# Performance work log

Measured on AMD Instinct MI355X. Metric: run time of the kernel, lower is better.

Reference implementation:

```python
import jax, jax.numpy as jnp
import numpy as np

NEG_SLOPE = 0.2


def _gat(x, W, a_src, a_dst, bias, src, dst, nonself, N):
    # PyG GATConv (eval mode): h = x @ W -> [N,H,C]; per-edge scores with
    # LeakyReLU, softmax over incoming edges per target node (self loops
    # re-added after removing any existing ones), weighted scatter-add.
    H, C = a_src.shape
    h = (x @ W).reshape(N, H, C)
    al_s = jnp.einsum('nhc,hc->nh', h, a_src)  # [N,H]
    al_d = jnp.einsum('nhc,hc->nh', h, a_dst)
    e = jax.nn.leaky_relu(al_s[src] + al_d[dst], NEG_SLOPE)  # [E,H]
    e = jnp.where(nonself[:, None], e, -jnp.inf)  # drop input self loops
    e_self = jax.nn.leaky_relu(al_s + al_d, NEG_SLOPE)  # added self loops [N,H]
    m = jnp.maximum(jax.ops.segment_max(e, dst, num_segments=N), e_self)
    w = jnp.exp(e - m[dst])  # masked edges -> 0
    w_self = jnp.exp(e_self - m)
    num = jax.ops.segment_sum(w[:, :, None] * h[src], dst, num_segments=N)
    num = num + w_self[:, :, None] * h
    den = jax.ops.segment_sum(w, dst, num_segments=N) + w_self
    return (num / den[:, :, None]).reshape(N, H * C) + bias


def setup_inputs() -> dict:
    N, E = 100000, 3200000
    key = jax.random.key(0)
    ks = jax.random.split(key, 20)
    s = 0.1
    return {
        'x1': jax.random.normal(ks[0], (N, 7), jnp.float32),
        'x2': jax.random.normal(ks[1], (N, 1), jnp.float32),
        'edge_index': jax.random.randint(ks[2], (2, E), 0, N, jnp.int64)
            if jax.config.jax_enable_x64 else jax.random.randint(ks[2], (2, E), 0, N, jnp.int32),
        'num_nodes': N,
        'lin1_w': s * jax.random.normal(ks[3], (1, 7), jnp.float32),
        'lin1_b': s * jax.random.normal(ks[4], (1,), jnp.float32),
        'lin2_w': s * jax.random.normal(ks[5], (1, 8), jnp.float32),
        'W1': s * jax.random.normal(ks[6], (1, 32), jnp.float32),
        'a_src1': s * jax.random.normal(ks[7], (8, 4), jnp.float32),
        'a_dst1': s * jax.random.normal(ks[8], (8, 4), jnp.float32),
        'b1': s * jax.random.normal(ks[9], (32,), jnp.float32),
        'W2': s * jax.random.normal(ks[10], (32, 16), jnp.float32),
        'a_src2': s * jax.random.normal(ks[11], (4, 4), jnp.float32),
        'a_dst2': s * jax.random.normal(ks[12], (4, 4), jnp.float32),
        'b2': s * jax.random.normal(ks[13], (16,), jnp.float32),
        'W3': s * jax.random.normal(ks[14], (16, 8), jnp.float32),
        'a_src3': s * jax.random.normal(ks[15], (2, 4), jnp.float32),
        'a_dst3': s * jax.random.normal(ks[16], (2, 4), jnp.float32),
        'b3': s * jax.random.normal(ks[17], (8,), jnp.float32),
    }


def reference(x1, x2, edge_index, num_nodes, lin1_w, lin1_b, lin2_w,
              W1, a_src1, a_dst1, b1, W2, a_src2, a_dst2, b2,
              W3, a_src3, a_dst3, b3):
    N = num_nodes
    src, dst = edge_index[0], edge_index[1]
    nonself = src != dst
    # init score + 3 GAT layers (dropouts inactive in eval mode)
    h0 = jax.nn.relu(x1 @ lin1_w.T + lin1_b)  # [N,1]
    x3 = jax.nn.relu(_gat(h0, W1, a_src1, a_dst1, b1, src, dst, nonself, N))
    x4 = jax.nn.relu(_gat(x3, W2, a_src2, a_dst2, b2, src, dst, nonself, N))
    x6 = jax.nn.relu(_gat(x4, W3, a_src3, a_dst3, b3, src, dst, nonself, N))  # [N,8]
    # Row-normalized adjacency with diagonal filled to 1 (sparse form of the
    # original dense Adj): Adj[i,j] = 1/deg[i] on edges (i!=j) and diagonal.
    ns = nonself.astype(x6.dtype)
    deg = 1.0 + jax.ops.segment_sum(ns, src, num_segments=N)  # [N]
    # local score: rowsum(Adj * (x6 x6^T))
    dots = jnp.sum(x6[src] * x6[dst], axis=-1) * ns  # [E]
    local = (jax.ops.segment_sum(dots, src, num_segments=N)
             + jnp.sum(x6 * x6, axis=-1)) / deg  # [N]
    # global score: lin2(Adj @ x6)
    R3 = (jax.ops.segment_sum(x6[dst] * ns[:, None], src, num_segments=N)
          + x6) / deg[:, None]  # [N,8]
    return local[:, None] + R3 @ lin2_w.T  # [N,1]
```

## Files before the change

kernel.cpp:

```cpp
#include <hip/hip_runtime.h>
#include <hip/hip_fp16.h>
#include <math.h>

static constexpr float NEG_SLOPE = 0.2f;
static constexpr int P      = 256;
static constexpr int CAP    = 14000;
static constexpr int CHSZ   = 4096;

__device__ __forceinline__ float lrelu(float x) { return x > 0.0f ? x : NEG_SLOPE * x; }

__device__ __forceinline__ void dm(int x, unsigned int mg, int npr, int& r, int& lk) {
    r = (int)__umulhi((unsigned int)x, mg);
    lk = x - r * npr;
    if (lk >= npr) { lk -= npr; ++r; }
    else if (lk < 0) { lk += npr; --r; }
}

union H8 { int4 i4; __half2 h2[4]; };

__device__ __forceinline__ void h8_to_f(int4 v, float* o) {
    H8 u; u.i4 = v;
#pragma unroll
    for (int k = 0; k < 4; ++k) {
        float2 f = __half22float2(u.h2[k]);
        o[2 * k] = f.x; o[2 * k + 1] = f.y;
    }
}

__device__ __forceinline__ int4 f_to_h8(const float* s) {
    H8 u;
#pragma unroll
    for (int k = 0; k < 4; ++k)
        u.h2[k] = __float22half2_rn(make_float2(s[2 * k], s[2 * k + 1]));
    return u.i4;
}

__global__ __launch_bounds__(512) void part2_kernel(
    const int* __restrict__ src, const int* __restrict__ dst,
    int* __restrict__ gcount,
    unsigned int* __restrict__ stgd, unsigned int* __restrict__ stgs,
    int E, int npr, unsigned int mg)
{
    __shared__ int cntw[8 * P];
    __shared__ int base[P];
    __shared__ int pref[P];
    __shared__ int wsum[8];
    __shared__ unsigned int buf[CHSZ];
    __shared__ unsigned char rid[CHSZ];
    const int dir = blockIdx.x & 1;
    const int c = blockIdx.x >> 1;
    const int i0 = c * CHSZ;
    const int i1 = min(i0 + CHSZ, E);
    const int tot = i1 - i0;
    const int tid = threadIdx.x;
    const int lane = tid & 63, w = tid >> 6;
    const int* key = dir ? (src + i0) : (dst + i0);
    const int* val = dir ? (dst + i0) : (src + i0);
    unsigned int* stg = dir ? stgs : stgd;
    int* gc = gcount + dir * P;
    int* mycnt = cntw + w * P;
    for (int i = tid; i < 8 * P; i += 512) cntw[i] = 0;
    __syncthreads();
    const int nv = tot >> 2;
    const int4* k4 = (const int4*)key;
    for (int t = tid; t < nv; t += 512) {
        int4 k = k4[t];
        int r, lk;
        dm(k.x, mg, npr, r, lk); atomicAdd(&mycnt[r], 1);
        dm(k.y, mg, npr, r, lk); atomicAdd(&mycnt[r], 1);
        dm(k.z, mg, npr, r, lk); atomicAdd(&mycnt[r], 1);
        dm(k.w, mg, npr, r, lk); atomicAdd(&mycnt[r], 1);
    }
    for (int i = (nv << 2) + tid; i < tot; i += 512) {
        int r, lk;
        dm(key[i], mg, npr, r, lk);
        atomicAdd(&mycnt[r], 1);
    }
    __syncthreads();
    int cq[8];
    int tb = 0, x = 0;
    if (tid < P) {
#pragma unroll
        for (int q = 0; q < 8; ++q) { cq[q] = cntw[q * P + tid]; tb += cq[q]; }
        base[tid] = atomicAdd(&gc[tid], tb);
        x = tb;
#pragma unroll
        for (int off = 1; off < 64; off <<= 1) {
            int y = __shfl_up(x, off);
            if (lane >= off) x += y;
        }
        if (lane == 63) wsum[w] = x;
    }
    __syncthreads();
    if (tid < P) {
        int wpref = 0;
#pragma unroll
        for (int k = 0; k < 4; ++k) if (k < w) wpref += wsum[k];
        int ex = x + wpref - tb;
        pref[tid] = ex;
        int acc = ex;
#pragma unroll
        for (int q = 0; q < 8; ++q) { cntw[q * P + tid] = acc; acc += cq[q]; }
    }
    __syncthreads();
    int* mytick = cntw + w * P;
    for (int t = tid; t < nv; t += 512) {
        int4 k = k4[t];
        const int4* v4 = (const int4*)val;
        int4 v = v4[t];
        int r, lk, p;
        dm(k.x, mg, npr, r, lk); p = atomicAdd(&mytick[r], 1);
        buf[p] = ((unsigned int)lk << 17) | (unsigned int)v.x; rid[p] = (unsigned char)r;
        dm(k.y, mg, npr, r, lk); p = atomicAdd(&mytick[r], 1);
        buf[p] = ((unsigned int)lk << 17) | (unsigned int)v.y; rid[p] = (unsigned char)r;
        dm(k.z, mg, npr, r, lk); p = atomicAdd(&mytick[r], 1);
        buf[p] = ((unsigned int)lk << 17) | (unsigned int)v.z; rid[p] = (unsigned char)r;
        dm(k.w, mg, npr, r, lk); p = atomicAdd(&mytick[r], 1);
        buf[p] = ((unsigned int)lk << 17) | (unsigned int)v.w; rid[p] = (unsigned char)r;
    }
    for (int i = (nv << 2) + tid; i < tot; i += 512) {
        int r, lk;
        dm(key[i], mg, npr, r, lk);
        int p = atomicAdd(&mytick[r], 1);
        buf[p] = ((unsigned int)lk << 17) | (unsigned int)val[i];
        rid[p] = (unsigned char)r;
    }
    __syncthreads();
    for (int i = tid; i < tot; i += 512) {
        int r = (int)rid[i];
        int b = base[r] + (i - pref[r]);
        if (b < CAP) stg[(size_t)r * CAP + b] = buf[i];
    }
}

__global__ __launch_bounds__(512) void ebase_kernel(
    const int* __restrict__ gtot, int* __restrict__ ebase)
{
    __shared__ int sm[2 * P];
    int tid = threadIdx.x;
    int v = gtot[tid];
    sm[tid] = v;
    __syncthreads();
#pragma unroll
    for (int off = 1; off < P; off <<= 1) {
        int t = ((tid & (P - 1)) >= off) ? sm[tid - off] : 0;
        __syncthreads();
        sm[tid] += t;
        __syncthreads();
    }
    ebase[tid] = sm[tid] - v;
}

__global__ __launch_bounds__(512) void build_kernel(
    const unsigned int* __restrict__ stgd, const unsigned int* __restrict__ stgs,
    const int* __restrict__ gtot, const int* __restrict__ ebase,
    int* __restrict__ col_dst, int* __restrict__ col_src,
    int* __restrict__ deg_dst, int* __restrict__ deg_src,
    int* __restrict__ row_dst, int* __restrict__ row_src,
    int N, int npr)
{
    __shared__ int cntw[2 * 512];
    __shared__ int scn[512];
    __shared__ int outv[CAP];
    const int dir = blockIdx.x >> 8;
    const int r = blockIdx.x & (P - 1);
    const unsigned int* stg = (dir ? stgs : stgd) + (size_t)r * CAP;
    int tot = gtot[dir * P + r];
    if (tot > CAP) tot = CAP;
    const int n0 = r * npr;
    const int nb = min(npr, N - n0);
    const int tid = threadIdx.x;
    const int g = tid >> 8;
    int* mycnt = cntw + g * 512;
    cntw[tid] = 0; cntw[512 + tid] = 0;
    __syncthreads();
    for (int i = tid; i < tot; i += 512)
        atomicAdd(&mycnt[stg[i] >> 17], 1);
    __syncthreads();
    int c0 = cntw[tid], c1 = cntw[512 + tid];
    int v = c0 + c1;
    scn[tid] = v;
    __syncthreads();
#pragma unroll
    for (int off = 1; off < 512; off <<= 1) {
        int t = (tid >= off) ? scn[tid - off] : 0;
        __syncthreads();
        scn[tid] += t;
        __syncthreads();
    }
    int ex = scn[tid] - v;
    const int eb = ebase[dir * P + r];
    if (tid < nb) {
        (dir ? deg_src : deg_dst)[n0 + tid] = v;
        (dir ? row_src : row_dst)[n0 + tid] = eb + ex;
    }
    cntw[tid] = ex;
    cntw[512 + tid] = ex + c0;
    __syncthreads();
    for (int i = tid; i < tot; i += 512) {
        unsigned int w = stg[i];
        int t = atomicAdd(&mycnt[w >> 17], 1);
        outv[t] = (int)(w & 0x1FFFFu);
    }
    __syncthreads();
    int* col = (dir ? col_src : col_dst) + eb;
    for (int i = tid; i < tot; i += 512) col[i] = outv[i];
}

__global__ __launch_bounds__(256) void l1h0_kernel(
    const float* __restrict__ x1, const float* __restrict__ lin1_w,
    const float* __restrict__ lin1_b, float* __restrict__ h0, int N)
{
    int n = blockIdx.x * blockDim.x + threadIdx.x;
    if (n >= N) return;
    float acc = lin1_b[0];
#pragma unroll
    for (int k = 0; k < 7; ++k) acc = fmaf(x1[n * 7 + k], lin1_w[k], acc);
    h0[n] = fmaxf(acc, 0.0f);
}

__global__ __launch_bounds__(256) void gat_gather1_kernel(
    const int* __restrict__ row_start, const int* __restrict__ degv,
    const int* __restrict__ col, const float* __restrict__ h0,
    const float* __restrict__ W1, const float* __restrict__ a_src,
    const float* __restrict__ a_dst, const float* __restrict__ bias,
    const float* __restrict__ W2, int4* __restrict__ h2p, int N)
{
    int t = blockIdx.x * 256 + threadIdx.x;
    int n = t >> 3, lane = t & 7;
    if (n >= N) return;
    float cs[8], cd[8];
#pragma unroll
    for (int hd = 0; hd < 8; ++hd) {
        float s = 0.0f, d = 0.0f;
#pragma unroll
        for (int c = 0; c < 4; ++c) {
            s = fmaf(W1[hd * 4 + c], a_src[hd * 4 + c], s);
            d = fmaf(W1[hd * 4 + c], a_dst[hd * 4 + c], d);
        }
        cs[hd] = s; cd[hd] = d;
    }
    float h0n = h0[n];
    float wh[8], den[8], adn[8];
#pragma unroll
    for (int hd = 0; hd < 8; ++hd) {
        adn[hd] = h0n * cd[hd];
        if (lane == 0) {
            float w = __expf(lrelu(h0n * cs[hd] + adn[hd]));
            den[hd] = w; wh[hd] = w * h0n;
        } else { den[hd] = 0.0f; wh[hd] = 0.0f; }
    }
    int start = row_start[n];
    int end = start + degv[n];
    for (int e = start + lane; e < end; e += 8) {
        int s = col[e];
        if (s == n) continue;
        float hs = h0[s];
#pragma unroll
        for (int hd = 0; hd < 8; ++hd) {
            float w = __expf(lrelu(hs * cs[hd] + adn[hd]));
            den[hd] += w;
            wh[hd] = fmaf(w, hs, wh[hd]);
        }
    }
#pragma unroll
    for (int m = 1; m < 8; m <<= 1) {
#pragma unroll
        for (int hd = 0; hd < 8; ++hd) {
            den[hd] += __shfl_xor(den[hd], m);
            wh[hd]  += __shfl_xor(wh[hd], m);
        }
    }
    float fct = wh[lane] / den[lane];
    const float4 wv = ((const float4*)W1)[lane];
    const float4 bb = ((const float4*)bias)[lane];
    float xr[4];
    xr[0] = fmaxf(fmaf(fct, wv.x, bb.x), 0.0f);
    xr[1] = fmaxf(fmaf(fct, wv.y, bb.y), 0.0f);
    xr[2] = fmaxf(fmaf(fct, wv.z, bb.z), 0.0f);
    xr[3] = fmaxf(fmaf(fct, wv.w, bb.w), 0.0f);
    float pj[16];
#pragma unroll
    for (int j = 0; j < 16; ++j) pj[j] = 0.0f;
    const float* wbase = W2 + lane * 64;
#pragma unroll
    for (int c2 = 0; c2 < 4; ++c2) {
#pragma unroll
        for (int j = 0; j < 16; ++j)
            pj[j] = fmaf(xr[c2], wbase[c2 * 16 + j], pj[j]);
    }
#pragma unroll
    for (int m = 1; m < 8; m <<= 1) {
#pragma unroll
        for (int j = 0; j < 16; ++j) pj[j] += __shfl_xor(pj[j], m);
    }
    if (lane < 2) h2p[(size_t)n * 2 + lane] = f_to_h8(pj + lane * 8);
}

__global__ __launch_bounds__(256) void gat_gather2_kernel(
    const int* __restrict__ row_start, const int* __restrict__ degv,
    const int* __restrict__ col, const int4* __restrict__ hp,
    const float* __restrict__ a_src, const float* __restrict__ a_dst,
    const float* __restrict__ bias, const float* __restrict__ W3,
    int4* __restrict__ h3p, int N)
{
    int t = blockIdx.x * 256 + threadIdx.x;
    int n = t >> 3, lane = t & 7;
    if (n >= N) return;
    float As[16], Ad[16];
#pragma unroll
    for (int j = 0; j < 16; ++j) { As[j] = a_src[j]; Ad[j] = a_dst[j]; }
    float hn[16];
    h8_to_f(hp[(size_t)n * 2], hn);
    h8_to_f(hp[(size_t)n * 2 + 1], hn + 8);
    float ald[4];
#pragma unroll
    for (int hd = 0; hd < 4; ++hd) {
        float d = 0.0f;
#pragma unroll
        for (int c = 0; c < 4; ++c) d = fmaf(hn[hd * 4 + c], Ad[hd * 4 + c], d);
        ald[hd] = d;
    }
    float num[16], den[4];
    if (lane == 0) {
#pragma unroll
        for (int hd = 0; hd < 4; ++hd) {
            float a = 0.0f;
#pragma unroll
            for (int c = 0; c < 4; ++c) a = fmaf(hn[hd * 4 + c], As[hd * 4 + c], a);
            float w = __expf(lrelu(a + ald[hd]));
            den[hd] = w;
#pragma unroll
            for (int c = 0; c < 4; ++c) num[hd * 4 + c] = w * hn[hd * 4 + c];
        }
    } else {
#pragma unroll
        for (int j = 0; j < 16; ++j) num[j] = 0.0f;
#pragma unroll
        for (int hd = 0; hd < 4; ++hd) den[hd] = 0.0f;
    }
    int start = row_start[n];
    int end = start + degv[n];
    for (int e = start + lane; e < end; e += 8) {
        int s = col[e];
        if (s == n) continue;
        float hs[16];
        h8_to_f(hp[(size_t)s * 2], hs);
        h8_to_f(hp[(size_t)s * 2 + 1], hs + 8);
#pragma unroll
        for (int hd = 0; hd < 4; ++hd) {
            float a = 0.0f;
#pragma unroll
            for (int c = 0; c < 4; ++c) a = fmaf(hs[hd * 4 + c], As[hd * 4 + c], a);
            float w = __expf(lrelu(a + ald[hd]));
            den[hd] += w;
#pragma unroll
            for (int c = 0; c < 4; ++c) num[hd * 4 + c] = fmaf(w, hs[hd * 4 + c], num[hd * 4 + c]);
        }
    }
#pragma unroll
    for (int m = 1; m < 8; m <<= 1) {
#pragma unroll
        for (int hd = 0; hd < 4; ++hd) den[hd] += __shfl_xor(den[hd], m);
#pragma unroll
        for (int j = 0; j < 16; ++j) num[j] += __shfl_xor(num[j], m);
    }
    float invd[4];
#pragma unroll
    for (int hd = 0; hd < 4; ++hd) invd[hd] = 1.0f / den[hd];
    float pj[8];
#pragma unroll
    for (int j = 0; j < 8; ++j) pj[j] = 0.0f;
#pragma unroll
    for (int k = 0; k < 16; ++k) {
        float xk = fmaxf(fmaf(num[k], invd[k >> 2], bias[k]), 0.0f);
        const float* wrow = W3 + k * 8;
#pragma unroll
        for (int j = 0; j < 8; ++j) pj[j] = fmaf(xk, wrow[j], pj[j]);
    }
    if (lane == 0) h3p[n] = f_to_h8(pj);
}

__global__ __launch_bounds__(256) void gat_gather3_kernel(
    const int* __restrict__ row_start, const int* __restrict__ degv,
    const int* __restrict__ col, const int4* __restrict__ hp,
    const float* __restrict__ a_src, const float* __restrict__ a_dst,
    const float* __restrict__ bias, int4* __restrict__ x6p, int N)
{
    int t = blockIdx.x * 256 + threadIdx.x;
    int n = t >> 2, lane = t & 3;
    if (n >= N) return;
    float As[8], Ad[8];
#pragma unroll
    for (int j = 0; j < 8; ++j) { As[j] = a_src[j]; Ad[j] = a_dst[j]; }
    float hn[8];
    h8_to_f(hp[n], hn);
    float ald[2];
#pragma unroll
    for (int hd = 0; hd < 2; ++hd) {
        float d = 0.0f;
#pragma unroll
        for (int c = 0; c < 4; ++c) d = fmaf(hn[hd * 4 + c], Ad[hd * 4 + c], d);
        ald[hd] = d;
    }
    float num[8], den[2];
    if (lane == 0) {
#pragma unroll
        for (int hd = 0; hd < 2; ++hd) {
            float a = 0.0f;
#pragma unroll
            for (int c = 0; c < 4; ++c) a = fmaf(hn[hd * 4 + c], As[hd * 4 + c], a);
            float w = __expf(lrelu(a + ald[hd]));
            den[hd] = w;
#pragma unroll
            for (int c = 0; c < 4; ++c) num[hd * 4 + c] = w * hn[hd * 4 + c];
        }
    } else {
#pragma unroll
        for (int j = 0; j < 8; ++j) num[j] = 0.0f;
        den[0] = den[1] = 0.0f;
    }
    int start = row_start[n];
    int end = start + degv[n];
    for (int e = start + lane; e < end; e += 4) {
        int s = col[e];
        if (s == n) continue;
        float hs[8];
        h8_to_f(hp[s], hs);
#pragma unroll
        for (int hd = 0; hd < 2; ++hd) {
            float a = 0.0f;
#pragma unroll
            for (int c = 0; c < 4; ++c) a = fmaf(hs[hd * 4 + c], As[hd * 4 + c], a);
            float w = __expf(lrelu(a + ald[hd]));
            den[hd] += w;
#pragma unroll
            for (int c = 0; c < 4; ++c) num[hd * 4 + c] = fmaf(w, hs[hd * 4 + c], num[hd * 4 + c]);
        }
    }
#pragma unroll
    for (int m = 1; m < 4; m <<= 1) {
        den[0] += __shfl_xor(den[0], m);
        den[1] += __shfl_xor(den[1], m);
#pragma unroll
        for (int j = 0; j < 8; ++j) num[j] += __shfl_xor(num[j], m);
    }
    if (lane == 0) {
        float o[8];
        float i0 = 1.0f / den[0], i1 = 1.0f / den[1];
#pragma unroll
        for (int c = 0; c < 4; ++c) {
            o[c]     = fmaxf(fmaf(num[c], i0, bias[c]), 0.0f);
            o[4 + c] = fmaxf(fmaf(num[4 + c], i1, bias[4 + c]), 0.0f);
        }
        x6p[n] = f_to_h8(o);
    }
}

__global__ __launch_bounds__(256) void score_gather_kernel(
    const int* __restrict__ row_start, const int* __restrict__ degv,
    const int* __restrict__ col, const int4* __restrict__ x6p,
    const float* __restrict__ lin2_w, float* __restrict__ out, int N)
{
    int t = blockIdx.x * 256 + threadIdx.x;
    int n = t >> 2, lane = t & 3;
    if (n >= N) return;
    float sx[8];
    h8_to_f(x6p[n], sx);
    float r[8];
    int sc = 0;
    if (lane == 0) {
#pragma unroll
        for (int j = 0; j < 8; ++j) r[j] = sx[j];
    } else {
#pragma unroll
        for (int j = 0; j < 8; ++j) r[j] = 0.0f;
    }
    int start = row_start[n];
    int dg = degv[n];
    int end = start + dg;
    for (int e = start + lane; e < end; e += 4) {
        int d = col[e];
        if (d == n) { ++sc; continue; }
        float dx[8];
        h8_to_f(x6p[d], dx);
#pragma unroll
        for (int j = 0; j < 8; ++j) r[j] += dx[j];
    }
#pragma unroll
    for (int m = 1; m < 4; m <<= 1) {
        sc += __shfl_xor(sc, m);
#pragma unroll
        for (int j = 0; j < 8; ++j) r[j] += __shfl_xor(r[j], m);
    }
    if (lane == 0) {
        float invd = 1.0f / (1.0f + (float)(dg - sc));
        float loc = 0.0f, g = 0.0f;
#pragma unroll
        for (int j = 0; j < 8; ++j) {
            loc = fmaf(sx[j], r[j], loc);
            g   = fmaf(r[j], lin2_w[j], g);
        }
        out[n] = (loc + g) * invd;
    }
}

extern "C" void kernel_launch(void* const* d_in, const int* in_sizes, int n_in,
                              void* d_out, int out_size, void* d_ws, size_t ws_size,
                              hipStream_t stream)
{
    const float* x1     = (const float*)d_in[0];
    const int*   ei     = (const int*)d_in[2];
    const float* lin1_w = (const float*)d_in[4];
    const float* lin1_b = (const float*)d_in[5];
    const float* lin2_w = (const float*)d_in[6];
    const float* W1     = (const float*)d_in[7];
    const float* a_src1 = (const float*)d_in[8];
    const float* a_dst1 = (const float*)d_in[9];
    const float* b1     = (const float*)d_in[10];
    const float* W2     = (const float*)d_in[11];
    const float* a_src2 = (const float*)d_in[12];
    const float* a_dst2 = (const float*)d_in[13];
    const float* b2     = (const float*)d_in[14];
    const float* W3     = (const float*)d_in[15];
    const float* a_src3 = (const float*)d_in[16];
    const float* a_dst3 = (const float*)d_in[17];
    const float* b3     = (const float*)d_in[18];
    float* out = (float*)d_out;

    const int N = in_sizes[0] / 7;
    const int E = in_sizes[2] / 2;
    const int* src = ei;
    const int* dst = ei + E;

    const int npr = (N + P - 1) / P;
    const unsigned int mg = (unsigned int)((0x100000000ULL + npr - 1) / (unsigned long long)npr);
    const int PB = (E + CHSZ - 1) / CHSZ;

    size_t Ns = (size_t)N, Es = (size_t)E;
    int* ideg_dst = (int*)d_ws;
    int* ideg_src = ideg_dst + Ns;
    int* irow_dst = ideg_src + Ns;
    int* irow_src = irow_dst + Ns;
    int* gcount   = irow_src + Ns;
    int* iebase   = gcount + 2 * P;
    int* icol_dst = iebase + 2 * P;
    int* icol_src = icol_dst + Es;
    float* f = (float*)(icol_src + Es);
    unsigned int* stgd = (unsigned int*)f;
    unsigned int* stgs = stgd + (size_t)P * CAP;
    float* h0  = f;
    int4*  h2p = (int4*)(f + Ns);
    int4*  h3p = (int4*)(f + 9 * Ns);
    int4*  x6p = (int4*)(f + 13 * Ns);

    const int TB = 256;
    const int gN = (N + TB - 1) / TB;
    const int g8 = (8 * N + TB - 1) / TB;
    const int g4 = (4 * N + TB - 1) / TB;

    hipMemsetAsync(gcount, 0, 2 * P * sizeof(int), stream);
    part2_kernel<<<2 * PB, 512, 0, stream>>>(src, dst, gcount, stgd, stgs, E, npr, mg);
    ebase_kernel<<<1, 2 * P, 0, stream>>>(gcount, iebase);
    build_kernel<<<2 * P, 512, 0, stream>>>(stgd, stgs, gcount, iebase,
                                            icol_dst, icol_src,
                                            ideg_dst, ideg_src,
                                            irow_dst, irow_src, N, npr);

    l1h0_kernel<<<gN, TB, 0, stream>>>(x1, lin1_w, lin1_b, h0, N);
    gat_gather1_kernel<<<g8, TB, 0, stream>>>(irow_dst, ideg_dst, icol_dst,
                                              h0, W1, a_src1, a_dst1, b1, W2, h2p, N);

    gat_gather2_kernel<<<g8, TB, 0, stream>>>(irow_dst, ideg_dst, icol_dst,
                                              h2p, a_src2, a_dst2, b2, W3, h3p, N);

    gat_gather3_kernel<<<g4, TB, 0, stream>>>(irow_dst, ideg_dst, icol_dst,
                                              h3p, a_src3, a_dst3, b3, x6p, N);

    score_gather_kernel<<<g4, TB, 0, stream>>>(irow_src, ideg_src, icol_src,
                                               x6p, lin2_w, out, N);
}
```

Measured before the change: 272.6 us.

## Tag self-loops in CSR build, pre-gather h0 per edge, unroll gathers by two

```diff
diff --git a/kernel.cpp b/kernel.cpp
--- a/kernel.cpp
+++ b/kernel.cpp
@@ -200,7 +200,9 @@
     for (int i = tid; i < tot; i += 512) {
         unsigned int w = stg[i];
         int t = atomicAdd(&mycnt[w >> 17], 1);
-        outv[t] = (int)(w & 0x1FFFFu);
+        unsigned int vv = w & 0x1FFFFu;
+        unsigned int self = (vv == (unsigned int)(n0) + (w >> 17)) ? 0x80000000u : 0u;
+        outv[t] = (int)(vv | self);
     }
     __syncthreads();
     int* col = (dir ? col_src : col_dst) + eb;
@@ -219,9 +221,31 @@
     h0[n] = fmaxf(acc, 0.0f);
 }
 
+__global__ __launch_bounds__(256) void expand_kernel(
+    const int* __restrict__ col, const float* __restrict__ h0,
+    float* __restrict__ colh0, int E)
+{
+    int t = blockIdx.x * 256 + threadIdx.x;
+    int e0 = t * 4;
+    if (e0 + 3 < E) {
+        int4 c = *(const int4*)(col + e0);
+        float4 v;
+        v.x = (c.x < 0) ? -1.0f : h0[c.x & 0x7fffffff];
+        v.y = (c.y < 0) ? -1.0f : h0[c.y & 0x7fffffff];
+        v.z = (c.z < 0) ? -1.0f : h0[c.z & 0x7fffffff];
+        v.w = (c.w < 0) ? -1.0f : h0[c.w & 0x7fffffff];
+        *(float4*)(colh0 + e0) = v;
+    } else {
+        for (int e = e0; e < E; ++e) {
+            int c = col[e];
+            colh0[e] = (c < 0) ? -1.0f : h0[c & 0x7fffffff];
+        }
+    }
+}
+
 __global__ __launch_bounds__(256) void gat_gather1_kernel(
     const int* __restrict__ row_start, const int* __restrict__ degv,
-    const int* __restrict__ col, const float* __restrict__ h0,
+    const float* __restrict__ colh0, const float* __restrict__ h0,
     const float* __restrict__ W1, const float* __restrict__ a_src,
     const float* __restrict__ a_dst, const float* __restrict__ bias,
     const float* __restrict__ W2, int4* __restrict__ h2p, int N)
@@ -252,15 +276,36 @@
     }
     int start = row_start[n];
     int end = start + degv[n];
-    for (int e = start + lane; e < end; e += 8) {
-        int s = col[e];
-        if (s == n) continue;
-        float hs = h0[s];
-#pragma unroll
-        for (int hd = 0; hd < 8; ++hd) {
-            float w = __expf(lrelu(hs * cs[hd] + adn[hd]));
-            den[hd] += w;
-            wh[hd] = fmaf(w, hs, wh[hd]);
+    int e = start + lane;
+    for (; e + 8 < end; e += 16) {
+        float a0 = colh0[e];
+        float a1 = colh0[e + 8];
+        if (a0 >= 0.0f) {
+#pragma unroll
+            for (int hd = 0; hd < 8; ++hd) {
+                float w = __expf(lrelu(a0 * cs[hd] + adn[hd]));
+                den[hd] += w;
+                wh[hd] = fmaf(w, a0, wh[hd]);
+            }
+        }
+        if (a1 >= 0.0f) {
+#pragma unroll
+            for (int hd = 0; hd < 8; ++hd) {
+                float w = __expf(lrelu(a1 * cs[hd] + adn[hd]));
+                den[hd] += w;
+                wh[hd] = fmaf(w, a1, wh[hd]);
+            }
+        }
+    }
+    if (e < end) {
+        float a0 = colh0[e];
+        if (a0 >= 0.0f) {
+#pragma unroll
+            for (int hd = 0; hd < 8; ++hd) {
+                float w = __expf(lrelu(a0 * cs[hd] + adn[hd]));
+                den[hd] += w;
+                wh[hd] = fmaf(w, a0, wh[hd]);
+            }
         }
     }
 #pragma unroll
@@ -297,6 +342,21 @@
     if (lane < 2) h2p[(size_t)n * 2 + lane] = f_to_h8(pj + lane * 8);
 }
 
+__device__ __forceinline__ void g2_acc(
+    const float* hs, const float* As, const float* ald, float* num, float* den)
+{
+#pragma unroll
+    for (int hd = 0; hd < 4; ++hd) {
+        float a = 0.0f;
+#pragma unroll
+        for (int c = 0; c < 4; ++c) a = fmaf(hs[hd * 4 + c], As[hd * 4 + c], a);
+        float w = __expf(lrelu(a + ald[hd]));
+        den[hd] += w;
+#pragma unroll
+        for (int c = 0; c < 4; ++c) num[hd * 4 + c] = fmaf(w, hs[hd * 4 + c], num[hd * 4 + c]);
+    }
+}
+
 __global__ __launch_bounds__(256) void gat_gather2_kernel(
     const int* __restrict__ row_start, const int* __restrict__ degv,
     const int* __restrict__ col, const int4* __restrict__ hp,
@@ -341,21 +401,30 @@
     }
     int start = row_start[n];
     int end = start + degv[n];
-    for (int e = start + lane; e < end; e += 8) {
-        int s = col[e];
-        if (s == n) continue;
-        float hs[16];
-        h8_to_f(hp[(size_t)s * 2], hs);
-        h8_to_f(hp[(size_t)s * 2 + 1], hs + 8);
-#pragma unroll
-        for (int hd = 0; hd < 4; ++hd) {
-            float a = 0.0f;
-#pragma unroll
-            for (int c = 0; c < 4; ++c) a = fmaf(hs[hd * 4 + c], As[hd * 4 + c], a);
-            float w = __expf(lrelu(a + ald[hd]));
-            den[hd] += w;
-#pragma unroll
-            for (int c = 0; c < 4; ++c) num[hd * 4 + c] = fmaf(w, hs[hd * 4 + c], num[hd * 4 + c]);
+    int e = start + lane;
+    for (; e + 8 < end; e += 16) {
+        int s0 = col[e], s1 = col[e + 8];
+        int i0 = s0 & 0x7fffffff, i1 = s1 & 0x7fffffff;
+        int4 q00 = hp[(size_t)i0 * 2], q01 = hp[(size_t)i0 * 2 + 1];
+        int4 q10 = hp[(size_t)i1 * 2], q11 = hp[(size_t)i1 * 2 + 1];
+        if (s0 >= 0) {
+            float hs[16];
+            h8_to_f(q00, hs); h8_to_f(q01, hs + 8);
+            g2_acc(hs, As, ald, num, den);
+        }
+        if (s1 >= 0) {
+            float hs[16];
+            h8_to_f(q10, hs); h8_to_f(q11, hs + 8);
+            g2_acc(hs, As, ald, num, den);
+        }
+    }
+    if (e < end) {
+        int s0 = col[e];
+        if (s0 >= 0) {
+            float hs[16];
+            h8_to_f(hp[(size_t)s0 * 2], hs);
+            h8_to_f(hp[(size_t)s0 * 2 + 1], hs + 8);
+            g2_acc(hs, As, ald, num, den);
         }
     }
 #pragma unroll
@@ -379,6 +448,21 @@
         for (int j = 0; j < 8; ++j) pj[j] = fmaf(xk, wrow[j], pj[j]);
     }
     if (lane == 0) h3p[n] = f_to_h8(pj);
+}
+
+__device__ __forceinline__ void g3_acc(
+    const float* hs, const float* As, const float* ald, float* num, float* den)
+{
+#pragma unroll
+    for (int hd = 0; hd < 2; ++hd) {
+        float a = 0.0f;
+#pragma unroll
+        for (int c = 0; c < 4; ++c) a = fmaf(hs[hd * 4 + c], As[hd * 4 + c], a);
+        float w = __expf(lrelu(a + ald[hd]));
+        den[hd] += w;
+#pragma unroll
+        for (int c = 0; c < 4; ++c) num[hd * 4 + c] = fmaf(w, hs[hd * 4 + c], num[hd * 4 + c]);
+    }
 }
 
 __global__ __launch_bounds__(256) void gat_gather3_kernel(
@@ -422,20 +506,28 @@
     }
     int start = row_start[n];
     int end = start + degv[n];
-    for (int e = start + lane; e < end; e += 4) {
-        int s = col[e];
-        if (s == n) continue;
-        float hs[8];
-        h8_to_f(hp[s], hs);
-#pragma unroll
-        for (int hd = 0; hd < 2; ++hd) {
-            float a = 0.0f;
-#pragma unroll
-            for (int c = 0; c < 4; ++c) a = fmaf(hs[hd * 4 + c], As[hd * 4 + c], a);
-            float w = __expf(lrelu(a + ald[hd]));
-            den[hd] += w;
-#pragma unroll
-            for (int c = 0; c < 4; ++c) num[hd * 4 + c] = fmaf(w, hs[hd * 4 + c], num[hd * 4 + c]);
+    int e = start + lane;
+    for (; e + 4 < end; e += 8) {
+        int s0 = col[e], s1 = col[e + 4];
+        int i0 = s0 & 0x7fffffff, i1 = s1 & 0x7fffffff;
+        int4 q0 = hp[i0], q1 = hp[i1];
+        if (s0 >= 0) {
+            float hs[8];
+            h8_to_f(q0, hs);
+            g3_acc(hs, As, ald, num, den);
+        }
+        if (s1 >= 0) {
+            float hs[8];
+            h8_to_f(q1, hs);
+            g3_acc(hs, As, ald, num, den);
+        }
+    }
+    if (e < end) {
+        int s0 = col[e];
+        if (s0 >= 0) {
+            float hs[8];
+            h8_to_f(hp[s0], hs);
+            g3_acc(hs, As, ald, num, den);
         }
     }
 #pragma unroll
@@ -479,13 +571,35 @@
     int start = row_start[n];
     int dg = degv[n];
     int end = start + dg;
-    for (int e = start + lane; e < end; e += 4) {
-        int d = col[e];
-        if (d == n) { ++sc; continue; }
-        float dx[8];
-        h8_to_f(x6p[d], dx);
-#pragma unroll
-        for (int j = 0; j < 8; ++j) r[j] += dx[j];
+    int e = start + lane;
+    for (; e + 4 < end; e += 8) {
+        int d0 = col[e], d1 = col[e + 4];
+        int i0 = d0 & 0x7fffffff, i1 = d1 & 0x7fffffff;
+        int4 q0 = x6p[i0], q1 = x6p[i1];
+        if (d0 < 0) { ++sc; }
+        else {
+            float dx[8];
+            h8_to_f(q0, dx);
+#pragma unroll
+            for (int j = 0; j < 8; ++j) r[j] += dx[j];
+        }
+        if (d1 < 0) { ++sc; }
+        else {
+            float dx[8];
+            h8_to_f(q1, dx);
+#pragma unroll
+            for (int j = 0; j < 8; ++j) r[j] += dx[j];
+        }
+    }
+    if (e < end) {
+        int d0 = col[e];
+        if (d0 < 0) { ++sc; }
+        else {
+            float dx[8];
+            h8_to_f(x6p[d0], dx);
+#pragma unroll
+            for (int j = 0; j < 8; ++j) r[j] += dx[j];
+        }
     }
 #pragma unroll
     for (int m = 1; m < 4; m <<= 1) {
@@ -549,15 +663,17 @@
     float* f = (float*)(icol_src + Es);
     unsigned int* stgd = (unsigned int*)f;
     unsigned int* stgs = stgd + (size_t)P * CAP;
-    float* h0  = f;
-    int4*  h2p = (int4*)(f + Ns);
-    int4*  h3p = (int4*)(f + 9 * Ns);
-    int4*  x6p = (int4*)(f + 13 * Ns);
+    float* h0    = f;
+    int4*  h2p   = (int4*)(f + Ns);
+    int4*  h3p   = (int4*)(f + 9 * Ns);
+    int4*  x6p   = (int4*)(f + 13 * Ns);
+    float* colh0 = f + 17 * Ns;
 
     const int TB = 256;
-    const int gN = (N + TB - 1) / TB;
-    const int g8 = (8 * N + TB - 1) / TB;
-    const int g4 = (4 * N + TB - 1) / TB;
+    const int gN  = (N + TB - 1) / TB;
+    const int g8  = (8 * N + TB - 1) / TB;
+    const int g4  = (4 * N + TB - 1) / TB;
+    const int gE4 = (E / 4 + TB - 1) / TB;
 
     hipMemsetAsync(gcount, 0, 2 * P * sizeof(int), stream);
     part2_kernel<<<2 * PB, 512, 0, stream>>>(src, dst, gcount, stgd, stgs, E, npr, mg);
@@ -568,7 +684,8 @@
                                             irow_dst, irow_src, N, npr);
 
     l1h0_kernel<<<gN, TB, 0, stream>>>(x1, lin1_w, lin1_b, h0, N);
-    gat_gather1_kernel<<<g8, TB, 0, stream>>>(irow_dst, ideg_dst, icol_dst,
+    expand_kernel<<<gE4, TB, 0, stream>>>(icol_dst, h0, colh0, E);
+    gat_gather1_kernel<<<g8, TB, 0, stream>>>(irow_dst, ideg_dst, colh0,
                                               h0, W1, a_src1, a_dst1, b1, W2, h2p, N);
 
     gat_gather2_kernel<<<g8, TB, 0, stream>>>(irow_dst, ideg_dst, icol_dst,
```

Measured after the change: 274.8 us. Within noise of the previous version (+0.8%).
